# Optimization experiments

Measured on AMD Instinct MI355X. Metric: run time of the kernel, lower is better.

Reference implementation:

```python
import jax, jax.numpy as jnp
import numpy as np

NUM_HEADS = 8
NUM_Q = 64
RANK = 64
DIM = 768
LN_EPS = 1e-5


def setup_inputs() -> dict:
    key = jax.random.key(0)
    ks = jax.random.split(key, 8)
    b, n = 4, 1024
    x = jax.random.normal(ks[0], (b, NUM_Q, DIM), dtype=jnp.float32)
    context = jax.random.normal(ks[1], (b, n, DIM), dtype=jnp.float32)
    s = 0.02
    Wq = jax.random.normal(ks[2], (DIM, DIM), dtype=jnp.float32) * s
    Wk = jax.random.normal(ks[3], (DIM, DIM), dtype=jnp.float32) * s
    Wv1 = jax.random.normal(ks[4], (DIM, NUM_Q * RANK), dtype=jnp.float32) * s
    ln_g = jnp.ones((NUM_Q * RANK,), dtype=jnp.float32)
    ln_b = jnp.zeros((NUM_Q * RANK,), dtype=jnp.float32)
    Wc = jax.random.normal(ks[5], (NUM_Q, RANK, DIM), dtype=jnp.float32) * s
    Wout = jax.random.normal(ks[6], (DIM, DIM), dtype=jnp.float32) * s
    return {"x": x, "context": context, "Wq": Wq, "Wk": Wk, "Wv1": Wv1,
            "ln_g": ln_g, "ln_b": ln_b, "Wc": Wc, "Wout": Wout}


def reference(x, context, Wq, Wk, Wv1, ln_g, ln_b, Wc, Wout):
    b, nq, d = x.shape
    n = context.shape[1]
    h, dh = NUM_HEADS, d // NUM_HEADS

    q = x @ Wq                      # [b, nq, d]
    k = context @ Wk                # [b, n, d]

    # q-aware V: Linear -> LayerNorm(all_q_mid) -> grouped 1x1 conv (per-query rank->d)
    h1 = context @ Wv1              # [b, n, NUM_Q*RANK]
    mu = jnp.mean(h1, axis=-1, keepdims=True)
    var = jnp.var(h1, axis=-1, keepdims=True)
    h1 = (h1 - mu) * jax.lax.rsqrt(var + LN_EPS) * ln_g + ln_b
    vmid = h1.reshape(b, n, NUM_Q, RANK)
    v = jnp.einsum('bnqr,qrd->bqnd', vmid, Wc)   # [b, NUM_Q, n, d]
    # split heads: 'b q n (h dh) -> b h q n dh'
    v = v.reshape(b, NUM_Q, n, h, dh).transpose(0, 3, 1, 2, 4)

    qh = q.reshape(b, nq, h, dh).transpose(0, 2, 1, 3)   # [b,h,nq,dh]
    kh = k.reshape(b, n, h, dh).transpose(0, 2, 1, 3)    # [b,h,n,dh]
    scale = dh ** (-0.25)
    sim = jnp.einsum('bhid,bhjd->bhij', qh * scale, kh * scale)
    attn = jax.nn.softmax(sim, axis=-1)                  # [b,h,nq,n]
    out = jnp.einsum('bhij,bhijd->bhid', attn, v)        # per-query V
    out = out.transpose(0, 2, 1, 3).reshape(b, nq, d)
    return out @ Wout
```

## Files before the change

kernel.cpp:

```cpp
#include <hip/hip_runtime.h>
#include <math.h>

typedef unsigned short ushort_t;
typedef __bf16 bf16x8 __attribute__((ext_vector_type(8)));
typedef float f32x4 __attribute__((ext_vector_type(4)));

__device__ __forceinline__ ushort_t f2b_rne(float f) {
    union { float f; unsigned int u; } c;
    c.f = f;
    unsigned int u = c.u;
    u += 0x7FFFu + ((u >> 16) & 1u);
    return (ushort_t)(u >> 16);
}
__device__ __forceinline__ float b2f(ushort_t v) {
    union { unsigned int u; float f; } c;
    c.u = ((unsigned int)v) << 16;
    return c.f;
}

__device__ __forceinline__ void gl_lds16(const ushort_t* g, ushort_t* l) {
    __builtin_amdgcn_global_load_lds(
        (const __attribute__((address_space(1))) void*)g,
        (__attribute__((address_space(3))) void*)l, 16, 0, 0);
}

__global__ __launch_bounds__(256) void prep(
    const float* __restrict__ x, const float* __restrict__ context,
    const float* __restrict__ Wq, const float* __restrict__ Wk,
    const float* __restrict__ Wv1, const float* __restrict__ Wout,
    ushort_t* __restrict__ x_b, ushort_t* __restrict__ ctx_b,
    ushort_t* __restrict__ Wq_t, ushort_t* __restrict__ Wk_t,
    ushort_t* __restrict__ Wv1_t, ushort_t* __restrict__ Wout_b,
    float* __restrict__ colzero,
    int b, int n) {
    const int t = threadIdx.x;
    const int bid = blockIdx.x;
    const int nb_x = (b * 64 * 768 / 4) / 256;
    const int nb_c = (b * n * 768 / 4) / 256;

    if (bid < nb_x + nb_c) {
        const float* in = (bid < nb_x) ? x : context;
        ushort_t* outp = (bid < nb_x) ? x_b : ctx_b;
        const int i = ((bid < nb_x) ? bid : (bid - nb_x)) * 256 + t;
        float4 v = ((const float4*)in)[i];
        ushort_t o[4] = {f2b_rne(v.x), f2b_rne(v.y), f2b_rne(v.z), f2b_rne(v.w)};
        *(uint2*)&outp[(size_t)i * 4] = *(uint2*)o;
        return;
    }

    int u = bid - nb_x - nb_c;
    if (u >= 4800) {
        const int idx = (u - 4800) * 256 + t;
        ((float4*)colzero)[idx] = make_float4(0.f, 0.f, 0.f, 0.f);
        return;
    }
    if (u >= 4224) {
        const int i = (u - 4224) * 256 + t;
        float4 v = ((const float4*)Wout)[i];
        ushort_t o[4] = {f2b_rne(v.x), f2b_rne(v.y), f2b_rne(v.z), f2b_rne(v.w)};
        *(uint2*)&Wout_b[(size_t)i * 4] = *(uint2*)o;
        return;
    }

    const float* in;
    ushort_t* outp;
    int R = 768, C = 768;
    if (u < 576)        { in = Wq;  outp = Wq_t; }
    else if (u < 1152)  { u -= 576;  in = Wk;  outp = Wk_t; }
    else                { u -= 1152; in = Wv1; outp = Wv1_t; C = 4096; }
    const int ct = C / 32;
    const int c0 = (u % ct) * 32, r0 = (u / ct) * 32;
    const int tx = t & 31, ty = t >> 5;

    __shared__ float tt[32][33];
#pragma unroll
    for (int i = 0; i < 4; i++)
        tt[ty + 8 * i][tx] = in[(size_t)(r0 + ty + 8 * i) * C + c0 + tx];
    __syncthreads();
#pragma unroll
    for (int i = 0; i < 4; i++)
        outp[(size_t)(c0 + ty + 8 * i) * R + r0 + tx] = f2b_rne(tt[tx][ty + 8 * i]);
}

template <int BM, int BN>
__device__ __forceinline__ void gemm_tile(
    const ushort_t* __restrict__ A, const ushort_t* __restrict__ Bt,
    ushort_t* __restrict__ C, int N, int row0, int col0, ushort_t* lds) {
    constexpr int K = 768;
    constexpr int NSTEP = 24;
    constexpr int SLOT = (BM + BN) * 32;
    constexpr int AW = BM / 128;
    constexpr int BW = BN / 128;
    constexpr int MI = BM / 32;
    constexpr int NJ = BN / 64;

    const int t = threadIdx.x;
    const int lane = t & 63, wave = t >> 6;
    const int quad = lane >> 4, l15 = lane & 15;
    const int wm = (wave >> 2) * (BM / 2);
    const int wn = (wave & 3) * (BN / 4);

    const int srow = lane >> 2;
    const int sslot = (lane & 3) ^ ((lane >> 3) & 3);
    const ushort_t* gA =
        A + (size_t)(row0 + wave * (AW * 16) + srow) * K + sslot * 8;
    const ushort_t* gB =
        Bt + (size_t)(col0 + wave * (BW * 16) + srow) * K + sslot * 8;
    const int ldsA = wave * (AW * 512);
    const int ldsB = BM * 32 + wave * (BW * 512);

    const int rslot = (quad ^ ((l15 >> 1) & 3)) * 8;
    const int abase = (wm + l15) * 32 + rslot;
    const int bbase = BM * 32 + (wn + l15) * 32 + rslot;

    f32x4 acc[MI][NJ] = {};

    auto STAGE = [&](int s) {
        const int rg = (s & 3) * SLOT;
        const int ko = s * 32;
        gl_lds16(gA + ko, lds + rg + ldsA);
        if constexpr (AW == 2) gl_lds16(gA + 16 * K + ko, lds + rg + ldsA + 512);
        gl_lds16(gB + ko, lds + rg + ldsB);
        if constexpr (BW == 2) gl_lds16(gB + 16 * K + ko, lds + rg + ldsB + 512);
    };

    auto COMPUTE = [&](int s) {
        const int rg = (s & 3) * SLOT;
        const ushort_t* pA = lds + rg + abase;
        const ushort_t* pB = lds + rg + bbase;
        bf16x8 af[MI], bfr[NJ];
#pragma unroll
        for (int i = 0; i < MI; ++i) af[i] = *(const bf16x8*)&pA[i * 512];
#pragma unroll
        for (int j = 0; j < NJ; ++j) bfr[j] = *(const bf16x8*)&pB[j * 512];
        __builtin_amdgcn_s_setprio(1);
#pragma unroll
        for (int i = 0; i < MI; ++i)
#pragma unroll
            for (int j = 0; j < NJ; ++j)
                acc[i][j] = __builtin_amdgcn_mfma_f32_16x16x32_bf16(
                    af[i], bfr[j], acc[i][j], 0, 0, 0);
        __builtin_amdgcn_s_setprio(0);
    };

    STAGE(0); STAGE(1); STAGE(2);

    for (int s = 0; s < NSTEP - 3; ++s) {
        __builtin_amdgcn_sched_barrier(0);
        __builtin_amdgcn_s_barrier();
        STAGE(s + 3);
        if constexpr (BM == 256)
            asm volatile("s_waitcnt vmcnt(12)" ::: "memory");
        else
            asm volatile("s_waitcnt vmcnt(6)" ::: "memory");
        __builtin_amdgcn_s_barrier();
        __builtin_amdgcn_sched_barrier(0);
        COMPUTE(s);
    }
    __builtin_amdgcn_sched_barrier(0);
    __builtin_amdgcn_s_barrier();
    if constexpr (BM == 256) asm volatile("s_waitcnt vmcnt(8)" ::: "memory");
    else                     asm volatile("s_waitcnt vmcnt(4)" ::: "memory");
    __builtin_amdgcn_s_barrier();
    __builtin_amdgcn_sched_barrier(0);
    COMPUTE(NSTEP - 3);

    __builtin_amdgcn_sched_barrier(0);
    __builtin_amdgcn_s_barrier();
    if constexpr (BM == 256) asm volatile("s_waitcnt vmcnt(4)" ::: "memory");
    else                     asm volatile("s_waitcnt vmcnt(2)" ::: "memory");
    __builtin_amdgcn_s_barrier();
    __builtin_amdgcn_sched_barrier(0);
    COMPUTE(NSTEP - 2);

    __builtin_amdgcn_sched_barrier(0);
    __builtin_amdgcn_s_barrier();
    asm volatile("s_waitcnt vmcnt(0)" ::: "memory");
    __builtin_amdgcn_s_barrier();
    __builtin_amdgcn_sched_barrier(0);
    COMPUTE(NSTEP - 1);

#pragma unroll
    for (int i = 0; i < MI; ++i)
#pragma unroll
        for (int j = 0; j < NJ; ++j)
#pragma unroll
            for (int r = 0; r < 4; ++r) {
                const int row = row0 + wm + i * 16 + quad * 4 + r;
                const int col = col0 + wn + j * 16 + l15;
                C[(size_t)row * N + col] = f2b_rne(acc[i][j][r]);
            }
}

__global__ __launch_bounds__(512, 2) void gemm_ring(
    const ushort_t* __restrict__ x_b, const ushort_t* __restrict__ ctx_b,
    const ushort_t* __restrict__ Wq_t, const ushort_t* __restrict__ Wk_t,
    const ushort_t* __restrict__ Wv1_t,
    ushort_t* __restrict__ qb, ushort_t* __restrict__ kb,
    ushort_t* __restrict__ h1t, int b, int n) {
    extern __shared__ ushort_t lds[];
    const int Mn = b * n;
    const int M = b * 64;
    const int nbig = 16 * (Mn / 256);
    const int nk = (Mn / 128) * 6;
    int u = blockIdx.x;
    if (u < nbig) {
        gemm_tile<256, 256>(Wv1_t, ctx_b, h1t, Mn,
                            (u & 15) * 256, (u >> 4) * 256, lds);
    } else if ((u -= nbig) < nk) {
        const int rt = Mn / 128;
        gemm_tile<128, 128>(ctx_b, Wk_t, kb, 768,
                            (u % rt) * 128, (u / rt) * 128, lds);
    } else {
        u -= nk;
        const int rt = M / 128;
        gemm_tile<128, 128>(x_b, Wq_t, qb, 768,
                            (u % rt) * 128, (u / rt) * 128, lds);
    }
}

__global__ __launch_bounds__(256) void scores_stats(
    const ushort_t* __restrict__ qb, const ushort_t* __restrict__ kb,
    const ushort_t* __restrict__ h1t, float* __restrict__ S,
    float* __restrict__ colsum, float* __restrict__ colsumsq,
    int b, int n, int Mn) {
    __shared__ ushort_t sb[192 * 104];
    const int t = threadIdx.x;
    const int nsc = b * 8 * (n / 128);

    if (blockIdx.x >= nsc) {
        const int u = blockIdx.x - nsc;
        const int rc = u >> 4;
        const int cc = u & 15;
        const int cg = t & 31;
        const int rg = t >> 5;
        const ushort_t* p =
            h1t + (size_t)(rc * 256 + rg * 32) * Mn + cc * 256 + cg * 8;
        float s[8] = {}, s2[8] = {};
#pragma unroll 4
        for (int r = 0; r < 32; r++) {
            const bf16x8 v = *(const bf16x8*)&p[(size_t)r * Mn];
#pragma unroll
            for (int j = 0; j < 8; j++) {
                const float f = (float)v[j];
                s[j] += f;
                s2[j] += f * f;
            }
        }
        float* red = (float*)sb;
#pragma unroll
        for (int j = 0; j < 8; j++) {
            red[rg * 256 + cg * 8 + j] = s[j];
            red[2048 + rg * 256 + cg * 8 + j] = s2[j];
        }
        __syncthreads();
        float ts = 0.f, ts2 = 0.f;
#pragma unroll
        for (int g = 0; g < 8; g++) {
            ts += red[g * 256 + t];
            ts2 += red[2048 + g * 256 + t];
        }
        atomicAdd(&colsum[cc * 256 + t], ts);
        atomicAdd(&colsumsq[cc * 256 + t], ts2);
        return;
    }

    const int nt = n / 128;
    const int n0 = (blockIdx.x % nt) * 128;
    const int bh = blockIdx.x / nt;
    const int bb = bh >> 3, h = bh & 7;
    const int lane = t & 63, wave = t >> 6;
    const int quad = lane >> 4, l15 = lane & 15;
    const int wm = (wave >> 1) * 32;
    const int wn = (wave & 1) * 64;

    ushort_t* Qs = sb;
    ushort_t* Ks = sb + 64 * 104;

    for (int g = t; g < 768; g += 256) {
        const int r = g / 12, s = g - r * 12;
        *(bf16x8*)&Qs[r * 104 + s * 8] =
            *(const bf16x8*)&qb[(size_t)(bb * 64 + r) * 768 + h * 96 + s * 8];
    }
    for (int g = t; g < 1536; g += 256) {
        const int r = g / 12, s = g - r * 12;
        *(bf16x8*)&Ks[r * 104 + s * 8] =
            *(const bf16x8*)&kb[(size_t)(bb * n + n0 + r) * 768 + h * 96 + s * 8];
    }
    __syncthreads();

    f32x4 acc[2][4] = {};
#pragma unroll
    for (int ks = 0; ks < 3; ks++) {
        bf16x8 af[2], bfr[4];
#pragma unroll
        for (int i = 0; i < 2; i++)
            af[i] = *(const bf16x8*)&Qs[(wm + i * 16 + l15) * 104 + ks * 32 + quad * 8];
#pragma unroll
        for (int j = 0; j < 4; j++)
            bfr[j] = *(const bf16x8*)&Ks[(wn + j * 16 + l15) * 104 + ks * 32 + quad * 8];
#pragma unroll
        for (int i = 0; i < 2; i++)
#pragma unroll
            for (int j = 0; j < 4; j++)
                acc[i][j] = __builtin_amdgcn_mfma_f32_16x16x32_bf16(
                    af[i], bfr[j], acc[i][j], 0, 0, 0);
    }

    const float sc = 0.10206207261596575f;
    float* Sp = S + (size_t)bh * 64 * n;
#pragma unroll
    for (int i = 0; i < 2; i++)
#pragma unroll
        for (int j = 0; j < 4; j++)
#pragma unroll
            for (int r = 0; r < 4; r++) {
                const int row = wm + i * 16 + quad * 4 + r;
                const int col = n0 + wn + j * 16 + l15;
                Sp[(size_t)row * n + col] = acc[i][j][r] * sc;
            }
}

__global__ __launch_bounds__(1024) void attn_fused(
    const float* __restrict__ S, const float* __restrict__ colsum,
    const float* __restrict__ colsumsq, const ushort_t* __restrict__ h1t,
    const float* __restrict__ ln_g, const float* __restrict__ ln_b,
    const float* __restrict__ Wc, const ushort_t* __restrict__ Wout_b,
    float* __restrict__ out, int n, int Mn) {
    const int bq = blockIdx.x;
    const int bb = bq >> 6, qi = bq & 63;
    const int tid = threadIdx.x;
    const int lane = tid & 63, wv = tid >> 6;
    const int quad = lane >> 4, l15 = lane & 15;

    __shared__ ushort_t sW[9 * 1032];
    __shared__ ushort_t sH[64 * 264];
    __shared__ float sl[8], swmu[8];
    __shared__ float pm[16], pl[16], pwm[16];
    __shared__ float sA[512];
    __shared__ float sO[768];

    float* sMu = (float*)sH;
    float* sRs = (float*)sH + 1024;

    for (int i = tid; i < n; i += 1024) {
        const float cs = colsum[bb * n + i];
        const float cq = colsumsq[bb * n + i];
        const float m = cs * (1.0f / 4096.0f);
        sMu[i] = m;
        sRs[i] = rsqrtf(cq * (1.0f / 4096.0f) - m * m + 1e-5f);
    }
    for (int i = tid; i < 1032; i += 1024) sW[8 * 1032 + i] = 0;
    __syncthreads();

    const int h = wv >> 1;
    const int half = wv & 1;
    const int nh = n >> 1;
    const int i0 = half * nh;
    const float* Sp = S + ((size_t)(bb * 8 + h) * 64 + qi) * n;
    {
        float m = -1e30f;
        for (int i = i0 + lane; i < i0 + nh; i += 64) m = fmaxf(m, Sp[i]);
#pragma unroll
        for (int off = 32; off > 0; off >>= 1) m = fmaxf(m, __shfl_down(m, off));
        if (lane == 0) pm[wv] = m;
    }
    __syncthreads();
    const float mh = fmaxf(pm[2 * h], pm[2 * h + 1]);
    {
        float l = 0.f, wm = 0.f;
        for (int i = i0 + lane; i < i0 + nh; i += 64) {
            const float e = expf(Sp[i] - mh);
            const float w = e * sRs[i];
            const ushort_t wb = f2b_rne(w);
            sW[h * 1032 + i] = wb;
            l += e;
            wm += b2f(wb) * sMu[i];
        }
#pragma unroll
        for (int off = 32; off > 0; off >>= 1) {
            l += __shfl_down(l, off);
            wm += __shfl_down(wm, off);
        }
        if (lane == 0) { pl[wv] = l; pwm[wv] = wm; }
    }
    __syncthreads();
    if (tid < 8) {
        sl[tid] = pl[2 * tid] + pl[2 * tid + 1];
        swmu[tid] = pwm[2 * tid] + pwm[2 * tid + 1];
    }

    const int mrow = (l15 < 8 ? l15 : 8) * 1032;
    f32x4 acc = {};
    const int nch = n >> 8;
    for (int ch = 0; ch < nch; ch++) {
        __syncthreads();
        for (int g = tid; g < 2048; g += 1024) {
            const int row = g >> 5, seg = g & 31;
            *(bf16x8*)&sH[row * 264 + seg * 8] =
                *(const bf16x8*)&h1t[(size_t)(qi * 64 + row) * Mn + bb * n +
                                     ch * 256 + seg * 8];
        }
        __syncthreads();
        if (wv < 4) {
#pragma unroll
            for (int ks = 0; ks < 8; ks++) {
                const bf16x8 af = *(const bf16x8*)&sW[mrow + ch * 256 + ks * 32 + quad * 8];
                const bf16x8 bf = *(const bf16x8*)&sH[(wv * 16 + l15) * 264 + ks * 32 + quad * 8];
                acc = __builtin_amdgcn_mfma_f32_16x16x32_bf16(af, bf, acc, 0, 0, 0);
            }
        }
    }
    __syncthreads();

    if (wv < 4) {
#pragma unroll
        for (int r = 0; r < 4; r++) {
            const int hh = quad * 4 + r;
            if (hh < 8) {
                const int rr = wv * 16 + l15;
                const int c = qi * 64 + rr;
                sA[hh * 64 + rr] =
                    ln_g[c] * ((acc[r] - swmu[hh]) / sl[hh]) + ln_b[c];
            }
        }
    }
    __syncthreads();

    for (int d = tid; d < 768; d += 1024) {
        const int hh = d / 96;
        const float* wp = Wc + (size_t)qi * 49152 + d;
        float a = 0.f;
#pragma unroll
        for (int r = 0; r < 64; r++) a += sA[hh * 64 + r] * wp[(size_t)r * 768];
        sO[d] = b2f(f2b_rne(a));
    }
    __syncthreads();

    float* rbuf = (float*)sH;
    if (tid < 768) {
        const int r0 = tid / 96;
        const int c0 = (tid % 96) * 8;
        const ushort_t* wp = Wout_b + (size_t)(r0 * 96) * 768 + c0;
        float acc8[8] = {};
#pragma unroll 4
        for (int s = 0; s < 96; s++) {
            const float sv = sO[r0 * 96 + s];
            const bf16x8 w8 = *(const bf16x8*)&wp[(size_t)s * 768];
#pragma unroll
            for (int j = 0; j < 8; j++) acc8[j] += sv * (float)w8[j];
        }
#pragma unroll
        for (int j = 0; j < 8; j++) rbuf[r0 * 768 + c0 + j] = acc8[j];
    }
    __syncthreads();
    if (tid < 768) {
        float s = 0.f;
#pragma unroll
        for (int g = 0; g < 8; g++) s += rbuf[g * 768 + tid];
        out[(size_t)bq * 768 + tid] = s;
    }
}

extern "C" void kernel_launch(void* const* d_in, const int* in_sizes, int n_in,
                              void* d_out, int out_size, void* d_ws, size_t ws_size,
                              hipStream_t stream) {
    const float* x       = (const float*)d_in[0];
    const float* context = (const float*)d_in[1];
    const float* Wq      = (const float*)d_in[2];
    const float* Wk      = (const float*)d_in[3];
    const float* Wv1     = (const float*)d_in[4];
    const float* ln_g    = (const float*)d_in[5];
    const float* ln_b    = (const float*)d_in[6];
    const float* Wc      = (const float*)d_in[7];
    const float* Wout    = (const float*)d_in[8];
    float* out = (float*)d_out;

    const int b = in_sizes[0] / (64 * 768);
    const int n = in_sizes[1] / (b * 768);
    const int M  = b * 64;
    const int Mn = b * n;

    float* ws = (float*)d_ws;
    size_t off = 0;
    float* S       = ws + off;  off += (size_t)b * 8 * 64 * n;
    float* colsum  = ws + off;  off += (size_t)Mn;
    float* colsumsq= ws + off;  off += (size_t)Mn;

    ushort_t* us = (ushort_t*)(ws + off);
    size_t uo = 0;
    ushort_t* x_b    = us + uo;  uo += (size_t)M * 768;
    ushort_t* ctx_b  = us + uo;  uo += (size_t)Mn * 768;
    ushort_t* qb     = us + uo;  uo += (size_t)M * 768;
    ushort_t* kb     = us + uo;  uo += (size_t)Mn * 768;
    ushort_t* h1t    = us + uo;  uo += (size_t)Mn * 4096;
    ushort_t* Wq_t   = us + uo;  uo += (size_t)768 * 768;
    ushort_t* Wk_t   = us + uo;  uo += (size_t)768 * 768;
    ushort_t* Wv1_t  = us + uo;  uo += (size_t)4096 * 768;
    ushort_t* Wout_b = us + uo;  uo += (size_t)768 * 768;

    const int nb_x = (M * 768 / 4) / 256;
    const int nb_c = (Mn * 768 / 4) / 256;
    prep<<<nb_x + nb_c + 4800 + 8, 256, 0, stream>>>(
        x, context, Wq, Wk, Wv1, Wout, x_b, ctx_b, Wq_t, Wk_t, Wv1_t, Wout_b,
        colsum, b, n);

    const int nbig = 16 * (Mn / 256);
    const int nk = (Mn / 128) * 6;
    const int nq = (M / 128) * 6;
    static bool attr_done = false;
    if (!attr_done) {
        (void)hipFuncSetAttribute(reinterpret_cast<const void*>(&gemm_ring),
                                  hipFuncAttributeMaxDynamicSharedMemorySize,
                                  131072);
        attr_done = true;
    }
    gemm_ring<<<nbig + nk + nq, 512, 131072, stream>>>(
        x_b, ctx_b, Wq_t, Wk_t, Wv1_t, qb, kb, h1t, b, n);

    scores_stats<<<b * 8 * (n / 128) + 256, 256, 0, stream>>>(
        qb, kb, h1t, S, colsum, colsumsq, b, n, Mn);

    attn_fused<<<M, 1024, 0, stream>>>(S, colsum, colsumsq, h1t, ln_g, ln_b,
                                       Wc, Wout_b, out, n, Mn);
}
```

Baseline: 169.1 us.

## Split big GEMM tile into half-step LDS reads interleaved with staged loads

Replaces the templated GEMM tile with separate big and small versions. The 256x256 tile now splits each k-step into two halves. It reads B plus the low A fragments, issues the A prefetch, runs the low MFMAs, then reads the high A fragments, issues the B prefetch and runs the high MFMAs. The aim is to overlap LDS reads and global-to-LDS loads with MFMA work and to cut register pressure from holding all fragments at once. The tail of both kernels is simplified to a single vmcnt(0) wait before the last three steps, at the cost of extra barriers per step and a less gradual drain.

```diff
diff --git a/kernel.cpp b/kernel.cpp
--- a/kernel.cpp
+++ b/kernel.cpp
@@ -82,62 +82,182 @@
         outp[(size_t)(c0 + ty + 8 * i) * R + r0 + tx] = f2b_rne(tt[tx][ty + 8 * i]);
 }
 
-template <int BM, int BN>
-__device__ __forceinline__ void gemm_tile(
+__device__ __forceinline__ void gemm_tile_big(
     const ushort_t* __restrict__ A, const ushort_t* __restrict__ Bt,
     ushort_t* __restrict__ C, int N, int row0, int col0, ushort_t* lds) {
     constexpr int K = 768;
     constexpr int NSTEP = 24;
-    constexpr int SLOT = (BM + BN) * 32;
-    constexpr int AW = BM / 128;
-    constexpr int BW = BN / 128;
-    constexpr int MI = BM / 32;
-    constexpr int NJ = BN / 64;
+    constexpr int SLOT = 512 * 32;
 
     const int t = threadIdx.x;
     const int lane = t & 63, wave = t >> 6;
     const int quad = lane >> 4, l15 = lane & 15;
-    const int wm = (wave >> 2) * (BM / 2);
-    const int wn = (wave & 3) * (BN / 4);
+    const int wm = (wave >> 2) * 128;
+    const int wn = (wave & 3) * 64;
 
     const int srow = lane >> 2;
     const int sslot = (lane & 3) ^ ((lane >> 3) & 3);
-    const ushort_t* gA =
-        A + (size_t)(row0 + wave * (AW * 16) + srow) * K + sslot * 8;
-    const ushort_t* gB =
-        Bt + (size_t)(col0 + wave * (BW * 16) + srow) * K + sslot * 8;
-    const int ldsA = wave * (AW * 512);
-    const int ldsB = BM * 32 + wave * (BW * 512);
+    const ushort_t* gA = A + (size_t)(row0 + wave * 32 + srow) * K + sslot * 8;
+    const ushort_t* gB = Bt + (size_t)(col0 + wave * 32 + srow) * K + sslot * 8;
+    const int ldsA = wave * 1024;
+    const int ldsB = 256 * 32 + wave * 1024;
 
     const int rslot = (quad ^ ((l15 >> 1) & 3)) * 8;
     const int abase = (wm + l15) * 32 + rslot;
-    const int bbase = BM * 32 + (wn + l15) * 32 + rslot;
-
-    f32x4 acc[MI][NJ] = {};
+    const int bbase = 256 * 32 + (wn + l15) * 32 + rslot;
+
+    f32x4 acc[8][4] = {};
+    bf16x8 af[8], bfr[4];
+
+    auto STAGE_A = [&](int s) {
+        const int rg = (s & 3) * SLOT;
+        const int ko = s * 32;
+        gl_lds16(gA + ko, lds + rg + ldsA);
+        gl_lds16(gA + 16 * K + ko, lds + rg + ldsA + 512);
+    };
+    auto STAGE_B = [&](int s) {
+        const int rg = (s & 3) * SLOT;
+        const int ko = s * 32;
+        gl_lds16(gB + ko, lds + rg + ldsB);
+        gl_lds16(gB + 16 * K + ko, lds + rg + ldsB + 512);
+    };
+    auto READ_B = [&](int s) {
+        const ushort_t* p = lds + (s & 3) * SLOT + bbase;
+#pragma unroll
+        for (int j = 0; j < 4; ++j) bfr[j] = *(const bf16x8*)&p[j * 512];
+    };
+    auto READ_A_LO = [&](int s) {
+        const ushort_t* p = lds + (s & 3) * SLOT + abase;
+#pragma unroll
+        for (int i = 0; i < 4; ++i) af[i] = *(const bf16x8*)&p[i * 512];
+    };
+    auto READ_A_HI = [&](int s) {
+        const ushort_t* p = lds + (s & 3) * SLOT + abase;
+#pragma unroll
+        for (int i = 4; i < 8; ++i) af[i] = *(const bf16x8*)&p[i * 512];
+    };
+    auto MFMA_LO = [&]() {
+        __builtin_amdgcn_s_setprio(1);
+#pragma unroll
+        for (int i = 0; i < 4; ++i)
+#pragma unroll
+            for (int j = 0; j < 4; ++j)
+                acc[i][j] = __builtin_amdgcn_mfma_f32_16x16x32_bf16(
+                    af[i], bfr[j], acc[i][j], 0, 0, 0);
+        __builtin_amdgcn_s_setprio(0);
+    };
+    auto MFMA_HI = [&]() {
+        __builtin_amdgcn_s_setprio(1);
+#pragma unroll
+        for (int i = 4; i < 8; ++i)
+#pragma unroll
+            for (int j = 0; j < 4; ++j)
+                acc[i][j] = __builtin_amdgcn_mfma_f32_16x16x32_bf16(
+                    af[i], bfr[j], acc[i][j], 0, 0, 0);
+        __builtin_amdgcn_s_setprio(0);
+    };
+
+    STAGE_A(0); STAGE_B(0);
+    STAGE_A(1); STAGE_B(1);
+    STAGE_A(2); STAGE_B(2);
+    asm volatile("s_waitcnt vmcnt(8)" ::: "memory");
+    __builtin_amdgcn_s_barrier();
+
+    for (int s = 0; s < NSTEP - 3; ++s) {
+        READ_B(s);
+        READ_A_LO(s);
+        STAGE_A(s + 3);
+        __builtin_amdgcn_sched_barrier(0);
+        __builtin_amdgcn_s_barrier();
+        asm volatile("s_waitcnt lgkmcnt(0)" ::: "memory");
+        __builtin_amdgcn_sched_barrier(0);
+        MFMA_LO();
+        __builtin_amdgcn_sched_barrier(0);
+        __builtin_amdgcn_s_barrier();
+        READ_A_HI(s);
+        STAGE_B(s + 3);
+        asm volatile("s_waitcnt vmcnt(8)" ::: "memory");
+        __builtin_amdgcn_sched_barrier(0);
+        __builtin_amdgcn_s_barrier();
+        asm volatile("s_waitcnt lgkmcnt(0)" ::: "memory");
+        __builtin_amdgcn_sched_barrier(0);
+        MFMA_HI();
+        __builtin_amdgcn_sched_barrier(0);
+        __builtin_amdgcn_s_barrier();
+    }
+
+    asm volatile("s_waitcnt vmcnt(0)" ::: "memory");
+    __builtin_amdgcn_s_barrier();
+#pragma unroll
+    for (int s = NSTEP - 3; s < NSTEP; ++s) {
+        READ_B(s);
+        READ_A_LO(s);
+        READ_A_HI(s);
+        asm volatile("s_waitcnt lgkmcnt(0)" ::: "memory");
+        __builtin_amdgcn_sched_barrier(0);
+        MFMA_LO();
+        MFMA_HI();
+    }
+
+#pragma unroll
+    for (int i = 0; i < 8; ++i)
+#pragma unroll
+        for (int j = 0; j < 4; ++j)
+#pragma unroll
+            for (int r = 0; r < 4; ++r) {
+                const int row = row0 + wm + i * 16 + quad * 4 + r;
+                const int col = col0 + wn + j * 16 + l15;
+                C[(size_t)row * N + col] = f2b_rne(acc[i][j][r]);
+            }
+}
+
+__device__ __forceinline__ void gemm_tile_small(
+    const ushort_t* __restrict__ A, const ushort_t* __restrict__ Bt,
+    ushort_t* __restrict__ C, int N, int row0, int col0, ushort_t* lds) {
+    constexpr int K = 768;
+    constexpr int NSTEP = 24;
+    constexpr int SLOT = 256 * 32;
+
+    const int t = threadIdx.x;
+    const int lane = t & 63, wave = t >> 6;
+    const int quad = lane >> 4, l15 = lane & 15;
+    const int wm = (wave >> 2) * 64;
+    const int wn = (wave & 3) * 32;
+
+    const int srow = lane >> 2;
+    const int sslot = (lane & 3) ^ ((lane >> 3) & 3);
+    const ushort_t* gA = A + (size_t)(row0 + wave * 16 + srow) * K + sslot * 8;
+    const ushort_t* gB = Bt + (size_t)(col0 + wave * 16 + srow) * K + sslot * 8;
+    const int ldsA = wave * 512;
+    const int ldsB = 128 * 32 + wave * 512;
+
+    const int rslot = (quad ^ ((l15 >> 1) & 3)) * 8;
+    const int abase = (wm + l15) * 32 + rslot;
+    const int bbase = 128 * 32 + (wn + l15) * 32 + rslot;
+
+    f32x4 acc[4][2] = {};
 
     auto STAGE = [&](int s) {
         const int rg = (s & 3) * SLOT;
         const int ko = s * 32;
         gl_lds16(gA + ko, lds + rg + ldsA);
-        if constexpr (AW == 2) gl_lds16(gA + 16 * K + ko, lds + rg + ldsA + 512);
         gl_lds16(gB + ko, lds + rg + ldsB);
-        if constexpr (BW == 2) gl_lds16(gB + 16 * K + ko, lds + rg + ldsB + 512);
     };
 
     auto COMPUTE = [&](int s) {
         const int rg = (s & 3) * SLOT;
         const ushort_t* pA = lds + rg + abase;
         const ushort_t* pB = lds + rg + bbase;
-        bf16x8 af[MI], bfr[NJ];
-#pragma unroll
-        for (int i = 0; i < MI; ++i) af[i] = *(const bf16x8*)&pA[i * 512];
-#pragma unroll
-        for (int j = 0; j < NJ; ++j) bfr[j] = *(const bf16x8*)&pB[j * 512];
+        bf16x8 af[4], bfr[2];
+#pragma unroll
+        for (int i = 0; i < 4; ++i) af[i] = *(const bf16x8*)&pA[i * 512];
+#pragma unroll
+        for (int j = 0; j < 2; ++j) bfr[j] = *(const bf16x8*)&pB[j * 512];
         __builtin_amdgcn_s_setprio(1);
 #pragma unroll
-        for (int i = 0; i < MI; ++i)
-#pragma unroll
-            for (int j = 0; j < NJ; ++j)
+        for (int i = 0; i < 4; ++i)
+#pragma unroll
+            for (int j = 0; j < 2; ++j)
                 acc[i][j] = __builtin_amdgcn_mfma_f32_16x16x32_bf16(
                     af[i], bfr[j], acc[i][j], 0, 0, 0);
         __builtin_amdgcn_s_setprio(0);
@@ -149,41 +269,24 @@
         __builtin_amdgcn_sched_barrier(0);
         __builtin_amdgcn_s_barrier();
         STAGE(s + 3);
-        if constexpr (BM == 256)
-            asm volatile("s_waitcnt vmcnt(12)" ::: "memory");
-        else
-            asm volatile("s_waitcnt vmcnt(6)" ::: "memory");
+        asm volatile("s_waitcnt vmcnt(6)" ::: "memory");
         __builtin_amdgcn_s_barrier();
         __builtin_amdgcn_sched_barrier(0);
         COMPUTE(s);
     }
-    __builtin_amdgcn_sched_barrier(0);
-    __builtin_amdgcn_s_barrier();
-    if constexpr (BM == 256) asm volatile("s_waitcnt vmcnt(8)" ::: "memory");
-    else                     asm volatile("s_waitcnt vmcnt(4)" ::: "memory");
-    __builtin_amdgcn_s_barrier();
-    __builtin_amdgcn_sched_barrier(0);
-    COMPUTE(NSTEP - 3);
-
-    __builtin_amdgcn_sched_barrier(0);
-    __builtin_amdgcn_s_barrier();
-    if constexpr (BM == 256) asm volatile("s_waitcnt vmcnt(4)" ::: "memory");
-    else                     asm volatile("s_waitcnt vmcnt(2)" ::: "memory");
-    __builtin_amdgcn_s_barrier();
-    __builtin_amdgcn_sched_barrier(0);
-    COMPUTE(NSTEP - 2);
-
     __builtin_amdgcn_sched_barrier(0);
     __builtin_amdgcn_s_barrier();
     asm volatile("s_waitcnt vmcnt(0)" ::: "memory");
     __builtin_amdgcn_s_barrier();
     __builtin_amdgcn_sched_barrier(0);
+    COMPUTE(NSTEP - 3);
+    COMPUTE(NSTEP - 2);
     COMPUTE(NSTEP - 1);
 
 #pragma unroll
-    for (int i = 0; i < MI; ++i)
-#pragma unroll
-        for (int j = 0; j < NJ; ++j)
+    for (int i = 0; i < 4; ++i)
+#pragma unroll
+        for (int j = 0; j < 2; ++j)
 #pragma unroll
             for (int r = 0; r < 4; ++r) {
                 const int row = row0 + wm + i * 16 + quad * 4 + r;
@@ -205,17 +308,17 @@
     const int nk = (Mn / 128) * 6;
     int u = blockIdx.x;
     if (u < nbig) {
-        gemm_tile<256, 256>(Wv1_t, ctx_b, h1t, Mn,
-                            (u & 15) * 256, (u >> 4) * 256, lds);
+        gemm_tile_big(Wv1_t, ctx_b, h1t, Mn, (u & 15) * 256, (u >> 4) * 256,
+                      lds);
     } else if ((u -= nbig) < nk) {
         const int rt = Mn / 128;
-        gemm_tile<128, 128>(ctx_b, Wk_t, kb, 768,
-                            (u % rt) * 128, (u / rt) * 128, lds);
+        gemm_tile_small(ctx_b, Wk_t, kb, 768, (u % rt) * 128, (u / rt) * 128,
+                        lds);
     } else {
         u -= nk;
         const int rt = M / 128;
-        gemm_tile<128, 128>(x_b, Wq_t, qb, 768,
-                            (u % rt) * 128, (u / rt) * 128, lds);
+        gemm_tile_small(x_b, Wq_t, qb, 768, (u % rt) * 128, (u / rt) * 128,
+                        lds);
     }
 }
 
```

Result: no change. 167.6 us (-0.9%).
